# Optimization experiments

Measured on AMD Instinct MI355X. Metric: run time of the kernel, lower is better.

## Reference

```python
import jax, jax.numpy as jnp
import numpy as np

HIDDEN = 2048
HEADS = 16
HEAD_DIM = HIDDEN // HEADS  # 128
ROPE_BASE = 10000.0
RMS_EPS = 1e-6
MINUS_INF = -10000.0


def rms_norm(x, w):
    xf = x.astype(jnp.float32)
    var = jnp.mean(xf * xf, axis=-1, keepdims=True)
    return w * (x * jax.lax.rsqrt(var + RMS_EPS))


def rotate_half(x):
    x1, x2 = jnp.split(x, 2, axis=-1)
    return jnp.concatenate((-x2, x1), axis=-1)


def rope_tables(seq_len, dtype):
    inv_freq = 1.0 / (ROPE_BASE ** (jnp.arange(0, HEAD_DIM, 2, dtype=jnp.float32) / HEAD_DIM))
    t = jnp.arange(seq_len, dtype=jnp.float32)
    freqs = jnp.einsum('i,j->ij', t, inv_freq)           # [S, D/2]
    emb = jnp.concatenate((freqs, freqs), axis=-1)       # [S, D]
    return jnp.cos(emb).astype(dtype), jnp.sin(emb).astype(dtype)


def setup_inputs() -> dict:
    key = jax.random.key(0)
    ks = jax.random.split(key, 6)
    B, S, H = 2, 2048, HIDDEN
    x = jax.random.normal(ks[0], (B, S, H), dtype=jnp.float32) * 0.5
    norm_w = jnp.ones((H,), dtype=jnp.float32)
    scale = 0.02
    wq = jax.random.normal(ks[1], (H, H), dtype=jnp.float32) * scale
    wk = jax.random.normal(ks[2], (H, H), dtype=jnp.float32) * scale
    wv = jax.random.normal(ks[3], (H, H), dtype=jnp.float32) * scale
    wo = jax.random.normal(ks[4], (H, H), dtype=jnp.float32) * scale
    position_ids = jnp.broadcast_to(jnp.arange(S, dtype=jnp.int32), (B, S))
    return {"x": x, "norm_w": norm_w, "wq": wq, "wk": wk, "wv": wv,
            "wo": wo, "position_ids": position_ids}


def reference(x, norm_w, wq, wk, wv, wo, position_ids):
    B, S, H = x.shape
    h = rms_norm(x, norm_w)
    # torch Linear: y = h @ W.T, weight is [out, in]
    def proj(w):
        return jnp.einsum('bsd,od->bso', h, w).reshape(B, S, HEADS, HEAD_DIM).transpose(0, 2, 1, 3)
    q, k, v = proj(wq), proj(wk), proj(wv)  # [B, Hh, S, D]
    cos, sin = rope_tables(S, x.dtype)
    cos = cos[position_ids][:, None]  # [B, 1, S, D]
    sin = sin[position_ids][:, None]
    q = q * cos + rotate_half(q) * sin
    k = k * cos + rotate_half(k) * sin
    scores = jnp.einsum('bhqd,bhkd->bhqk', q, k) / jnp.sqrt(jnp.float32(HEAD_DIM))
    causal = jnp.tril(jnp.ones((S, S), dtype=bool))
    scores = scores + jnp.where(causal, 0.0, MINUS_INF).astype(scores.dtype)
    probs = jax.nn.softmax(scores, axis=-1)
    ctx = jnp.einsum('bhqk,bhkd->bhqd', probs, v)          # [B, Hh, S, D]
    ctx = ctx.transpose(0, 2, 1, 3).reshape(B, S, H)
    out = jnp.einsum('bsd,od->bso', ctx, wo)
    return out
```

## Files before the change

### kernel.cpp

```cpp
#include <hip/hip_runtime.h>
#include <hip/hip_bf16.h>
#include <stdint.h>

#define S_LEN   2048
#define BATCH   2
#define HID     2048
#define NHEADS  16
#define HDIM    128
#define ROWS    (BATCH * S_LEN)
#define QKS     4096
#define ATT_SCALE 0.08838834764831843f
#define LOG2E     1.4426950408889634f

typedef __attribute__((ext_vector_type(8))) short s16x8;
typedef __attribute__((ext_vector_type(4))) float f32x4;

#define GLL16(gp, lp)                                                          \
  __builtin_amdgcn_global_load_lds(                                            \
      (__attribute__((address_space(1))) void*)(gp),                           \
      (__attribute__((address_space(3))) void*)(lp), 16, 0, 0)

__device__ __forceinline__ float bf2f(unsigned short u) {
  union { unsigned int i; float f; } v; v.i = ((unsigned int)u) << 16; return v.f;
}
__device__ __forceinline__ unsigned short f2bf(float f) {
  union { float f; unsigned int i; } v; v.f = f;
  unsigned int i = v.i;
  return (unsigned short)((i + 0x7FFFu + ((i >> 16) & 1u)) >> 16);
}
__device__ __forceinline__ void store_out(unsigned short* p, float v) { *p = f2bf(v); }
__device__ __forceinline__ void store_out(float* p, float v) { *p = v; }

__global__ __launch_bounds__(256) void cast4_kernel(const float* __restrict__ w0,
                                                    const float* __restrict__ w1,
                                                    const float* __restrict__ w2,
                                                    const float* __restrict__ w3,
                                                    unsigned short* __restrict__ dqkv,
                                                    unsigned short* __restrict__ dwo) {
  const int which = blockIdx.y;
  const float* src = (which == 0) ? w0 : (which == 1) ? w1 : (which == 2) ? w2 : w3;
  unsigned short* dst = (which < 3) ? dqkv + (size_t)which * HID * HID : dwo;
  int i = blockIdx.x * 256 + threadIdx.x;
  float4 v = ((const float4*)src)[i];
  ushort4 o;
  o.x = f2bf(v.x); o.y = f2bf(v.y); o.z = f2bf(v.z); o.w = f2bf(v.w);
  ((ushort4*)dst)[i] = o;
}

__global__ __launch_bounds__(256) void rmsnorm_kernel(const float* __restrict__ x,
                                                      const float* __restrict__ w,
                                                      unsigned short* __restrict__ h) {
  int row = blockIdx.x;
  int t = threadIdx.x;
  const float4* xr4 = (const float4*)(x + (size_t)row * HID);
  float4 a = xr4[t], b = xr4[t + 256];
  float ss = a.x*a.x + a.y*a.y + a.z*a.z + a.w*a.w
           + b.x*b.x + b.y*b.y + b.z*b.z + b.w*b.w;
#pragma unroll
  for (int off = 32; off >= 1; off >>= 1) ss += __shfl_xor(ss, off, 64);
  __shared__ float red[4];
  if ((t & 63) == 0) red[t >> 6] = ss;
  __syncthreads();
  float tot = red[0] + red[1] + red[2] + red[3];
  float rs = rsqrtf(tot * (1.0f / (float)HID) + 1e-6f);
  const float4* w4 = (const float4*)w;
  float4 wa = w4[t], wb = w4[t + 256];
  ushort4 oa, ob;
  oa.x = f2bf(a.x * wa.x * rs); oa.y = f2bf(a.y * wa.y * rs);
  oa.z = f2bf(a.z * wa.z * rs); oa.w = f2bf(a.w * wa.w * rs);
  ob.x = f2bf(b.x * wb.x * rs); ob.y = f2bf(b.y * wb.y * rs);
  ob.z = f2bf(b.z * wb.z * rs); ob.w = f2bf(b.w * wb.w * rs);
  ushort4* hr = (ushort4*)(h + (size_t)row * HID);
  hr[t] = oa; hr[t + 256] = ob;
}

__global__ void rope_tab_kernel(float* __restrict__ cost, float* __restrict__ sint) {
  int s = blockIdx.x, j = threadIdx.x;
  float inv = powf(10000.0f, -((float)j) / 64.0f);
  float ang = (float)s * inv;
  cost[s * 64 + j] = cosf(ang);
  sint[s * 64 + j] = sinf(ang);
}

__global__ __launch_bounds__(256) void rope_kernel(const int* __restrict__ pos_ids,
                                                   const float* __restrict__ cost,
                                                   const float* __restrict__ sint,
                                                   unsigned short* __restrict__ qk) {
  int row = blockIdx.x;
  int p = pos_ids[row];
  int t = threadIdx.x;
  int head = t >> 4;
  int j0 = (t & 15) * 4;
  size_t base = (size_t)row * QKS + head * HDIM;
  float4 c = *(const float4*)(cost + p * 64 + j0);
  float4 s = *(const float4*)(sint + p * 64 + j0);
#pragma unroll
  for (int which = 0; which < 2; which++) {
    unsigned short* ptr = qk + base + which * HID;
    float sc = which ? 1.0f : (ATT_SCALE * LOG2E);
    ushort4 v1 = *(ushort4*)(ptr + j0);
    ushort4 v2 = *(ushort4*)(ptr + 64 + j0);
    ushort4 o1, o2;
    o1.x = f2bf((bf2f(v1.x) * c.x - bf2f(v2.x) * s.x) * sc);
    o1.y = f2bf((bf2f(v1.y) * c.y - bf2f(v2.y) * s.y) * sc);
    o1.z = f2bf((bf2f(v1.z) * c.z - bf2f(v2.z) * s.z) * sc);
    o1.w = f2bf((bf2f(v1.w) * c.w - bf2f(v2.w) * s.w) * sc);
    o2.x = f2bf((bf2f(v2.x) * c.x + bf2f(v1.x) * s.x) * sc);
    o2.y = f2bf((bf2f(v2.y) * c.y + bf2f(v1.y) * s.y) * sc);
    o2.z = f2bf((bf2f(v2.z) * c.z + bf2f(v1.z) * s.z) * sc);
    o2.w = f2bf((bf2f(v2.w) * c.w + bf2f(v1.w) * s.w) * sc);
    *(ushort4*)(ptr + j0) = o1;
    *(ushort4*)(ptr + 64 + j0) = o2;
  }
}

#define SH(kt, bi, kk2) {                                                      \
    const unsigned short* sa_ = aQ + (size_t)(kt) * 64 + (kk2) * 32;           \
    const unsigned short* sb_ = bQ + (size_t)(kt) * 64 + (kk2) * 32;           \
    char* da_ = qsm + ((bi) * 2 + (kk2)) * 32768 + tid * 16;                   \
    GLL16(sa_, da_);                                                           \
    GLL16(sa_ + (size_t)128 * K, da_ + 8192);                                  \
    GLL16(sb_, da_ + 16384);                                                   \
    GLL16(sb_ + (size_t)128 * K, da_ + 16384 + 8192);                          \
  }

__global__ __launch_bounds__(512, 2) void gemm_qk_kernel(const unsigned short* __restrict__ A,
                                                         const unsigned short* __restrict__ B,
                                                         unsigned short* __restrict__ C,
                                                         int K, int N) {
  __shared__ __align__(16) unsigned short Qsm[2][2][2][256 * 32];
  const int bm = blockIdx.y, bn = blockIdx.x;
  const int tid = threadIdx.x;
  const int w = tid >> 6, wr = w >> 2, wc = w & 3;
  const int l = tid & 63, g = l >> 4, r = l & 15;
  const int KT = K >> 6;

  const int srow = tid >> 2;
  const int sg = (tid & 3) ^ ((tid >> 2) & 3) ^ ((tid >> 4) & 3);
  const unsigned short* aQ = A + (size_t)(bm * 256 + srow) * K + sg * 8;
  const unsigned short* bQ = B + (size_t)(bn * 256 + srow) * K + sg * 8;
  char* const qsm = (char*)Qsm;

  f32x4 zero = {0.f, 0.f, 0.f, 0.f};
  f32x4 acc[8][4];
#pragma unroll
  for (int mi = 0; mi < 8; mi++)
#pragma unroll
    for (int ni = 0; ni < 4; ni++) acc[mi][ni] = zero;

  const int ro = ((g ^ (r & 3) ^ ((r >> 2) & 3)) << 4);
  const int aOff = (wr * 128 + r) * 64 + ro;
  const int bOff = 16384 + (wc * 64 + r) * 64 + ro;

  SH(0, 0, 0); SH(0, 0, 1);

  for (int kt = 0; kt < KT; ++kt) {
    const int buf = kt & 1;
    const bool more = (kt + 1 < KT);
    const char* l0 = qsm + (buf * 2 + 0) * 32768;
    const char* l1 = qsm + (buf * 2 + 1) * 32768;

    asm volatile("s_waitcnt vmcnt(4)" ::: "memory");
    __builtin_amdgcn_s_barrier();
    __builtin_amdgcn_sched_barrier(0);
    s16x8 a[4], b[4];
#pragma unroll
    for (int ni = 0; ni < 4; ni++) b[ni] = *(const s16x8*)(l0 + bOff + ni * 1024);
#pragma unroll
    for (int i = 0; i < 4; i++) a[i] = *(const s16x8*)(l0 + aOff + i * 1024);
    if (more) SH(kt + 1, buf ^ 1, 0);
    __builtin_amdgcn_s_setprio(1);
#pragma unroll
    for (int ni = 0; ni < 4; ni++)
#pragma unroll
      for (int i = 0; i < 4; i++)
        acc[i][ni] = __builtin_amdgcn_mfma_f32_16x16x32_bf16(a[i], b[ni], acc[i][ni], 0, 0, 0);
    __builtin_amdgcn_s_setprio(0);

    s16x8 a2[4];
#pragma unroll
    for (int i = 0; i < 4; i++) a2[i] = *(const s16x8*)(l0 + aOff + (4 + i) * 1024);
    __builtin_amdgcn_s_setprio(1);
#pragma unroll
    for (int ni = 0; ni < 4; ni++)
#pragma unroll
      for (int i = 0; i < 4; i++)
        acc[4 + i][ni] = __builtin_amdgcn_mfma_f32_16x16x32_bf16(a2[i], b[ni], acc[4 + i][ni], 0, 0, 0);
    __builtin_amdgcn_s_setprio(0);

    if (more) { asm volatile("s_waitcnt vmcnt(4)" ::: "memory"); }
    else      { asm volatile("s_waitcnt vmcnt(0)" ::: "memory"); }
    __builtin_amdgcn_s_barrier();
    __builtin_amdgcn_sched_barrier(0);
#pragma unroll
    for (int ni = 0; ni < 4; ni++) b[ni] = *(const s16x8*)(l1 + bOff + ni * 1024);
#pragma unroll
    for (int i = 0; i < 4; i++) a[i] = *(const s16x8*)(l1 + aOff + i * 1024);
    if (more) SH(kt + 1, buf ^ 1, 1);
    __builtin_amdgcn_s_setprio(1);
#pragma unroll
    for (int ni = 0; ni < 4; ni++)
#pragma unroll
      for (int i = 0; i < 4; i++)
        acc[i][ni] = __builtin_amdgcn_mfma_f32_16x16x32_bf16(a[i], b[ni], acc[i][ni], 0, 0, 0);
    __builtin_amdgcn_s_setprio(0);

#pragma unroll
    for (int i = 0; i < 4; i++) a2[i] = *(const s16x8*)(l1 + aOff + (4 + i) * 1024);
    __builtin_amdgcn_s_setprio(1);
#pragma unroll
    for (int ni = 0; ni < 4; ni++)
#pragma unroll
      for (int i = 0; i < 4; i++)
        acc[4 + i][ni] = __builtin_amdgcn_mfma_f32_16x16x32_bf16(a2[i], b[ni], acc[4 + i][ni], 0, 0, 0);
    __builtin_amdgcn_s_setprio(0);
  }

#pragma unroll
  for (int mi = 0; mi < 8; mi++)
#pragma unroll
    for (int ni = 0; ni < 4; ni++) {
      const int crow = bm * 256 + wr * 128 + mi * 16 + g * 4;
      const int ccol = bn * 256 + wc * 64 + ni * 16 + r;
#pragma unroll
      for (int j = 0; j < 4; j++)
        store_out(&C[(size_t)(crow + j) * N + ccol], acc[mi][ni][j]);
    }
}
#undef SH

#define SA(kt, bi) {                                                           \
    const unsigned short* s_ = aS + (size_t)(kt) * 64;                         \
    char* d_ = (char*)Ab[bi] + tid * 16;                                       \
    GLL16(s_, d_);                                                             \
    GLL16(s_ + (size_t)64 * K, d_ + 8192);                                     \
  }
#define SB(kt, bi, hf) {                                                       \
    const unsigned short* s_ = bS + (size_t)(hf) * 128 * K + (size_t)(kt) * 64;\
    char* d_ = (char*)Bb[bi] + (hf) * 16384 + tid * 16;                        \
    GLL16(s_, d_);                                                             \
    GLL16(s_ + (size_t)64 * K, d_ + 8192);                                     \
  }

template <typename OutT, int NI, bool VT_OUT>
__global__ __launch_bounds__(512, 1) void gemm8_kernel(const unsigned short* __restrict__ A,
                                                       const unsigned short* __restrict__ B,
                                                       OutT* __restrict__ C, int K, int N) {
  __shared__ __align__(16) unsigned short Ab[3][128 * 64];
  __shared__ __align__(16) unsigned short Bb[3][NI * 64 * 64];
  const int bm = blockIdx.y, bn = blockIdx.x;
  const int tid = threadIdx.x;
  const int w = tid >> 6, wr = w >> 2, wc = w & 3;
  const int l = tid & 63, g = l >> 4, r = l & 15;
  const int KT = K >> 6;

  const int srow = tid >> 3;
  const int sgr = (tid & 7) ^ (srow & 7);
  const unsigned short* aS = A + (size_t)(bm * 128 + srow) * K + sgr * 8;
  const unsigned short* bS = B + (size_t)(bn * (NI * 64) + srow) * K + sgr * 8;

  f32x4 zero = {0.f, 0.f, 0.f, 0.f};
  f32x4 acc[4][NI];
#pragma unroll
  for (int mi = 0; mi < 4; mi++)
#pragma unroll
    for (int ni = 0; ni < NI; ni++) acc[mi][ni] = zero;

  const int swx = (r & 7) << 4;
  const int ks0 = (g << 4) ^ swx;
  const int ks1 = ((4 | g) << 4) ^ swx;
  const int aOff = (wr * 64 + r) * 128;
  const int bOff = (wc * (NI * 16) + r) * 128;

  SA(0, 0); SB(0, 0, 0); if (NI == 4) SB(0, 0, 1);
  SA(1, 1); SB(1, 1, 0); if (NI == 4) SB(1, 1, 1);

  int cur = 0;
  for (int kt = 0; kt < KT; ++kt) {
    const int b2 = (cur >= 1) ? cur - 1 : cur + 2;
    if (kt == KT - 1)      { asm volatile("s_waitcnt vmcnt(0)" ::: "memory"); }
    else if (NI == 4)      { asm volatile("s_waitcnt vmcnt(6)" ::: "memory"); }
    else                   { asm volatile("s_waitcnt vmcnt(4)" ::: "memory"); }
    __builtin_amdgcn_s_barrier();
    __builtin_amdgcn_sched_barrier(0);
    const char* lA = (const char*)Ab[cur];
    const char* lB = (const char*)Bb[cur];
    const bool more = (kt + 2 < KT);

    s16x8 a[4][2], b[NI][2];
#pragma unroll
    for (int mi = 0; mi < 4; mi++) {
      a[mi][0] = *(const s16x8*)(lA + aOff + mi * 2048 + ks0);
      a[mi][1] = *(const s16x8*)(lA + aOff + mi * 2048 + ks1);
    }
#pragma unroll
    for (int ni = 0; ni < NI / 2; ni++) {
      b[ni][0] = *(const s16x8*)(lB + bOff + ni * 2048 + ks0);
      b[ni][1] = *(const s16x8*)(lB + bOff + ni * 2048 + ks1);
    }
    if (more) { SA(kt + 2, b2); if (NI == 4) SB(kt + 2, b2, 0); }
    __builtin_amdgcn_s_setprio(1);
#pragma unroll
    for (int kk = 0; kk < 2; kk++)
#pragma unroll
      for (int ni = 0; ni < NI / 2; ni++)
#pragma unroll
        for (int mi = 0; mi < 4; mi++)
          acc[mi][ni] = __builtin_amdgcn_mfma_f32_16x16x32_bf16(a[mi][kk], b[ni][kk], acc[mi][ni], 0, 0, 0);
    __builtin_amdgcn_s_setprio(0);
    __builtin_amdgcn_sched_barrier(0);

#pragma unroll
    for (int ni = NI / 2; ni < NI; ni++) {
      b[ni][0] = *(const s16x8*)(lB + bOff + ni * 2048 + ks0);
      b[ni][1] = *(const s16x8*)(lB + bOff + ni * 2048 + ks1);
    }
    if (more) { if (NI == 4) { SB(kt + 2, b2, 1); } else { SB(kt + 2, b2, 0); } }
    __builtin_amdgcn_s_setprio(1);
#pragma unroll
    for (int kk = 0; kk < 2; kk++)
#pragma unroll
      for (int ni = NI / 2; ni < NI; ni++)
#pragma unroll
        for (int mi = 0; mi < 4; mi++)
          acc[mi][ni] = __builtin_amdgcn_mfma_f32_16x16x32_bf16(a[mi][kk], b[ni][kk], acc[mi][ni], 0, 0, 0);
    __builtin_amdgcn_s_setprio(0);
    cur = (cur == 2) ? 0 : cur + 1;
  }

#pragma unroll
  for (int mi = 0; mi < 4; mi++)
#pragma unroll
    for (int ni = 0; ni < NI; ni++) {
      const int crow = bm * 128 + wr * 64 + mi * 16 + g * 4;
      const int ccol = bn * (NI * 64) + wc * (NI * 16) + ni * 16 + r;
      if constexpr (VT_OUT) {
        const int bidx = crow >> 11;
        const int s0 = crow & (S_LEN - 1);
        const int vrow = (bidx * 16 + (ccol >> 7)) * 128 + (ccol & 127);
        ushort4 o;
        o.x = f2bf(acc[mi][ni][0]); o.y = f2bf(acc[mi][ni][1]);
        o.z = f2bf(acc[mi][ni][2]); o.w = f2bf(acc[mi][ni][3]);
        *(ushort4*)((unsigned short*)C + (size_t)vrow * S_LEN + s0) = o;
      } else {
#pragma unroll
        for (int j = 0; j < 4; j++)
          store_out(&C[(size_t)(crow + j) * N + ccol], acc[mi][ni][j]);
      }
    }
}

__global__ __launch_bounds__(256, 2) void attn_kernel(const unsigned short* __restrict__ QK,
                                                      const unsigned short* __restrict__ VT,
                                                      unsigned short* __restrict__ O) {
  __shared__ __align__(16) unsigned short Ksm[2][64 * 128];
  __shared__ __align__(16) unsigned short VTsm[2][128 * 64];
  __shared__ __align__(16) unsigned short Psm[4 * 16 * 64];
  const int bid = blockIdx.x;
  const int grp = bid & 7, idx = bid >> 3;
  const int p = idx >> 2;
  const int bh = (grp << 2) | (idx & 3);
  const int b = bh >> 4, hd = bh & 15;
  const int tid = threadIdx.x, w = tid >> 6, l = tid & 63, g = l >> 4, r = l & 15;

  const int cK = tid & 15, rowK = tid >> 4;
  const unsigned short* kp_base = QK + (size_t)(b * S_LEN + rowK) * QKS + HID + hd * HDIM
                                  + ((cK ^ (rowK & 7)) << 3);
  const int cV = tid & 7, dV = tid >> 3;
  const unsigned short* vp_base = VT + (size_t)(bh * 128 + dV) * S_LEN + ((cV ^ (dV & 7)) << 3);
  char* const ksm0 = (char*)Ksm;
  char* const vtsm0 = (char*)VTsm;
  char* const psm_w = (char*)Psm + w * 2048;
  const int pswz = (r & 7) << 4;
  f32x4 zero = {0.f, 0.f, 0.f, 0.f};

#define STAGE(kt, bufi)                                                        \
  {                                                                            \
    const unsigned short* kp_ = kp_base + (size_t)((kt) * 64) * QKS;           \
    const unsigned short* vp_ = vp_base + (kt) * 64;                           \
    char* kd_ = ksm0 + (bufi) * 16384;                                         \
    char* vd_ = vtsm0 + (bufi) * 16384;                                        \
    GLL16(kp_,                      kd_ + tid * 16);                           \
    GLL16(kp_ + (size_t)16 * QKS,   kd_ + (tid + 256) * 16);                   \
    GLL16(kp_ + (size_t)32 * QKS,   kd_ + (tid + 512) * 16);                   \
    GLL16(kp_ + (size_t)48 * QKS,   kd_ + (tid + 768) * 16);                   \
    GLL16(vp_,                      vd_ + tid * 16);                           \
    GLL16(vp_ + (size_t)32 * S_LEN, vd_ + (tid + 256) * 16);                   \
    GLL16(vp_ + (size_t)64 * S_LEN, vd_ + (tid + 512) * 16);                   \
    GLL16(vp_ + (size_t)96 * S_LEN, vd_ + (tid + 768) * 16);                   \
  }

  for (int pass = 0; pass < 2; pass++) {
    const int qt = pass ? p : 31 - p;
    const int qbs = qt * 64 + w * 16;

    const unsigned short* qp = QK + (size_t)(b * S_LEN + qbs + r) * QKS + hd * HDIM;
    s16x8 qf[4];
#pragma unroll
    for (int ks = 0; ks < 4; ks++) qf[ks] = *(const s16x8*)(qp + ks * 32 + g * 8);

    float mreg = -1e30f, lregp = 0.f;
    f32x4 oacc[8];
#pragma unroll
    for (int di = 0; di < 8; di++) oacc[di] = zero;

    if (pass) __builtin_amdgcn_s_barrier();
    const int nt = qt + 1;
    STAGE(0, 0);

    for (int kt2 = 0; kt2 < nt; kt2++) {
      const int buf = kt2 & 1;
      asm volatile("s_waitcnt vmcnt(0)" ::: "memory");
      __builtin_amdgcn_s_barrier();
      __builtin_amdgcn_sched_barrier(0);
      if (kt2 + 1 < nt) STAGE(kt2 + 1, buf ^ 1);

      const char* ksm_c = ksm0 + buf * 16384;
      const char* vtsm_c = vtsm0 + buf * 16384;

      f32x4 sacc[4];
#pragma unroll
      for (int ni = 0; ni < 4; ni++) sacc[ni] = zero;
#pragma unroll
      for (int ni = 0; ni < 4; ni++) {
        const int krow = ni * 16 + r;
        const int swz = (krow & 7) << 4;
        const char* kb2 = ksm_c + krow * 256;
#pragma unroll
        for (int ks = 0; ks < 4; ks++) {
          s16x8 kf = *(const s16x8*)(kb2 + ((ks * 64 + g * 16) ^ swz));
          sacc[ni] = __builtin_amdgcn_mfma_f32_16x16x32_bf16(kf, qf[ks], sacc[ni], 0, 0, 0);
        }
      }

      if (kt2 == qt) {
#pragma unroll
        for (int ni = 0; ni < 4; ni++)
#pragma unroll
          for (int jj = 0; jj < 4; jj++)
            if ((kt2 * 64 + ni * 16 + g * 4 + jj) > (qbs + r)) sacc[ni][jj] = -1e30f;
      }

      float m0 = fmaxf(fmaxf(sacc[0][0], sacc[0][1]), fmaxf(sacc[0][2], sacc[0][3]));
      float m1 = fmaxf(fmaxf(sacc[1][0], sacc[1][1]), fmaxf(sacc[1][2], sacc[1][3]));
      float m2 = fmaxf(fmaxf(sacc[2][0], sacc[2][1]), fmaxf(sacc[2][2], sacc[2][3]));
      float m3 = fmaxf(fmaxf(sacc[3][0], sacc[3][1]), fmaxf(sacc[3][2], sacc[3][3]));
      float mx = fmaxf(fmaxf(m0, m1), fmaxf(m2, m3));
      mx = fmaxf(mx, __shfl_xor(mx, 16, 64));
      mx = fmaxf(mx, __shfl_xor(mx, 32, 64));

      if (__any(mx > mreg + 8.0f)) {
        float mn = fmaxf(mreg, mx);
        float corr = exp2f(mreg - mn);
        mreg = mn;
        lregp *= corr;
#pragma unroll
        for (int di = 0; di < 8; di++) oacc[di] = oacc[di] * corr;
      }

#pragma unroll
      for (int ni = 0; ni < 4; ni++)
#pragma unroll
        for (int jj = 0; jj < 4; jj++) sacc[ni][jj] = exp2f(sacc[ni][jj] - mreg);
      float s0 = (sacc[0][0] + sacc[0][1]) + (sacc[0][2] + sacc[0][3]);
      float s1 = (sacc[1][0] + sacc[1][1]) + (sacc[1][2] + sacc[1][3]);
      float s2 = (sacc[2][0] + sacc[2][1]) + (sacc[2][2] + sacc[2][3]);
      float s3 = (sacc[3][0] + sacc[3][1]) + (sacc[3][2] + sacc[3][3]);
      lregp += (s0 + s1) + (s2 + s3);

#pragma unroll
      for (int ni = 0; ni < 4; ni++) {
        unsigned int pk01, pk23;
        asm("v_cvt_pk_bf16_f32 %0, %1, %2" : "=v"(pk01) : "v"(sacc[ni][0]), "v"(sacc[ni][1]));
        asm("v_cvt_pk_bf16_f32 %0, %1, %2" : "=v"(pk23) : "v"(sacc[ni][2]), "v"(sacc[ni][3]));
        uint2 pk; pk.x = pk01; pk.y = pk23;
        *(uint2*)(psm_w + ((r * 128 + ni * 32 + g * 8) ^ pswz)) = pk;
      }

#pragma unroll
      for (int ksl = 0; ksl < 2; ksl++) {
        s16x8 pb = *(const s16x8*)(psm_w + ((r * 128 + ksl * 64 + g * 16) ^ pswz));
        const int kgran = ksl * 4 + g;
#pragma unroll
        for (int di = 0; di < 8; di++) {
          const int d = di * 16 + r;
          s16x8 vf = *(const s16x8*)(vtsm_c + d * 128 + ((kgran ^ (d & 7)) << 4));
          oacc[di] = __builtin_amdgcn_mfma_f32_16x16x32_bf16(vf, pb, oacc[di], 0, 0, 0);
        }
      }
    }

    float lsum = lregp;
    lsum += __shfl_xor(lsum, 16, 64);
    lsum += __shfl_xor(lsum, 32, 64);
    const float inv = 1.0f / lsum;
    unsigned short* orow = O + (size_t)(b * S_LEN + qbs + r) * HID + hd * HDIM;
#pragma unroll
    for (int di = 0; di < 8; di++) {
      ushort4 o;
      o.x = f2bf(oacc[di][0] * inv); o.y = f2bf(oacc[di][1] * inv);
      o.z = f2bf(oacc[di][2] * inv); o.w = f2bf(oacc[di][3] * inv);
      *(ushort4*)(orow + di * 16 + g * 4) = o;
    }
  }
#undef STAGE
}

extern "C" void kernel_launch(void* const* d_in, const int* in_sizes, int n_in,
                              void* d_out, int out_size, void* d_ws, size_t ws_size,
                              hipStream_t stream) {
  const float* x      = (const float*)d_in[0];
  const float* norm_w = (const float*)d_in[1];
  const float* wq     = (const float*)d_in[2];
  const float* wk     = (const float*)d_in[3];
  const float* wv     = (const float*)d_in[4];
  const float* wo     = (const float*)d_in[5];
  const int*   pos    = (const int*)d_in[6];
  float* out = (float*)d_out;

  char* ws = (char*)d_ws;
  const size_t WQKV_B = (size_t)3 * HID * HID * 2;
  const size_t WO_B   = (size_t)HID * HID * 2;
  const size_t H_B    = (size_t)ROWS * HID * 2;
  const size_t QK_B   = (size_t)ROWS * QKS * 2;

  unsigned short* wqkvb = (unsigned short*)(ws);
  unsigned short* vt    = (unsigned short*)(ws);
  unsigned short* wob   = (unsigned short*)(ws + WQKV_B);
  unsigned short* h     = (unsigned short*)(ws + WQKV_B + WO_B);
  unsigned short* qk    = (unsigned short*)(ws + WQKV_B + WO_B + H_B);
  float* cost = (float*)(ws + WQKV_B + WO_B + H_B + QK_B);
  float* sint = cost + (size_t)S_LEN * 64;

  dim3 cgrid(HID * HID / 4 / 256, 4);
  cast4_kernel<<<cgrid, 256, 0, stream>>>(wq, wk, wv, wo, wqkvb, wob);
  rope_tab_kernel<<<S_LEN, 64, 0, stream>>>(cost, sint);
  rmsnorm_kernel<<<ROWS, 256, 0, stream>>>(x, norm_w, h);

  dim3 qkgrid(2 * HID / 256, ROWS / 256);
  gemm_qk_kernel<<<qkgrid, 512, 0, stream>>>(h, wqkvb, qk, HID, QKS);

  dim3 vgrid(HID / 256, ROWS / 128);
  gemm8_kernel<unsigned short, 4, true><<<vgrid, 512, 0, stream>>>(
      h, wqkvb + (size_t)2 * HID * HID, vt, HID, S_LEN);

  rope_kernel<<<ROWS, 256, 0, stream>>>(pos, cost, sint, qk);

  attn_kernel<<<512, 256, 0, stream>>>(qk, vt, h );

  dim3 ogrid(HID / 256, ROWS / 128);
  gemm8_kernel<float, 4, false><<<ogrid, 512, 0, stream>>>(h, wob, out, HID, HID);
}
```

Measured before the change: 255.3 us.

## Load V fragments straight into registers and launch one query tile per block

The attention kernel no longer stages the transposed V tile through double-buffered shared memory. Each wave now reads its V fragments directly from global memory into registers, issued right after the K prefetch, and feeds them to the PV MFMAs. Separately, the two-pass pairing of a long and a short query tile per block is replaced by 1024 blocks that each handle a single query tile, ordered heaviest first, and the launch-bounds occupancy hint is dropped. This frees shared memory and removes the V staging traffic, at the cost of four-fold redundant global (L2) reads of V across the waves in a block. It also adds more register pressure and leaves load balance to the hardware scheduler.

```diff
diff --git a/kernel.cpp b/kernel.cpp
--- a/kernel.cpp
+++ b/kernel.cpp
@@ -350,160 +350,149 @@
     }
 }
 
-__global__ __launch_bounds__(256, 2) void attn_kernel(const unsigned short* __restrict__ QK,
-                                                      const unsigned short* __restrict__ VT,
-                                                      unsigned short* __restrict__ O) {
+__global__ __launch_bounds__(256) void attn_kernel(const unsigned short* __restrict__ QK,
+                                                   const unsigned short* __restrict__ VT,
+                                                   unsigned short* __restrict__ O) {
   __shared__ __align__(16) unsigned short Ksm[2][64 * 128];
-  __shared__ __align__(16) unsigned short VTsm[2][128 * 64];
   __shared__ __align__(16) unsigned short Psm[4 * 16 * 64];
   const int bid = blockIdx.x;
   const int grp = bid & 7, idx = bid >> 3;
-  const int p = idx >> 2;
+  const int qt = 31 - (idx >> 2);
   const int bh = (grp << 2) | (idx & 3);
   const int b = bh >> 4, hd = bh & 15;
   const int tid = threadIdx.x, w = tid >> 6, l = tid & 63, g = l >> 4, r = l & 15;
+  const int qbs = qt * 64 + w * 16;
+
+  const unsigned short* qp = QK + (size_t)(b * S_LEN + qbs + r) * QKS + hd * HDIM;
+  s16x8 qf[4];
+#pragma unroll
+  for (int ks = 0; ks < 4; ks++) qf[ks] = *(const s16x8*)(qp + ks * 32 + g * 8);
+
+  float mreg = -1e30f, lregp = 0.f;
+  f32x4 zero = {0.f, 0.f, 0.f, 0.f};
+  f32x4 oacc[8];
+#pragma unroll
+  for (int di = 0; di < 8; di++) oacc[di] = zero;
 
   const int cK = tid & 15, rowK = tid >> 4;
   const unsigned short* kp_base = QK + (size_t)(b * S_LEN + rowK) * QKS + HID + hd * HDIM
                                   + ((cK ^ (rowK & 7)) << 3);
-  const int cV = tid & 7, dV = tid >> 3;
-  const unsigned short* vp_base = VT + (size_t)(bh * 128 + dV) * S_LEN + ((cV ^ (dV & 7)) << 3);
+  const unsigned short* vgp = VT + (size_t)(bh * 128 + r) * S_LEN + g * 8;
   char* const ksm0 = (char*)Ksm;
-  char* const vtsm0 = (char*)VTsm;
   char* const psm_w = (char*)Psm + w * 2048;
   const int pswz = (r & 7) << 4;
-  f32x4 zero = {0.f, 0.f, 0.f, 0.f};
 
 #define STAGE(kt, bufi)                                                        \
   {                                                                            \
     const unsigned short* kp_ = kp_base + (size_t)((kt) * 64) * QKS;           \
-    const unsigned short* vp_ = vp_base + (kt) * 64;                           \
     char* kd_ = ksm0 + (bufi) * 16384;                                         \
-    char* vd_ = vtsm0 + (bufi) * 16384;                                        \
     GLL16(kp_,                      kd_ + tid * 16);                           \
     GLL16(kp_ + (size_t)16 * QKS,   kd_ + (tid + 256) * 16);                   \
     GLL16(kp_ + (size_t)32 * QKS,   kd_ + (tid + 512) * 16);                   \
     GLL16(kp_ + (size_t)48 * QKS,   kd_ + (tid + 768) * 16);                   \
-    GLL16(vp_,                      vd_ + tid * 16);                           \
-    GLL16(vp_ + (size_t)32 * S_LEN, vd_ + (tid + 256) * 16);                   \
-    GLL16(vp_ + (size_t)64 * S_LEN, vd_ + (tid + 512) * 16);                   \
-    GLL16(vp_ + (size_t)96 * S_LEN, vd_ + (tid + 768) * 16);                   \
-  }
-
-  for (int pass = 0; pass < 2; pass++) {
-    const int qt = pass ? p : 31 - p;
-    const int qbs = qt * 64 + w * 16;
-
-    const unsigned short* qp = QK + (size_t)(b * S_LEN + qbs + r) * QKS + hd * HDIM;
-    s16x8 qf[4];
-#pragma unroll
-    for (int ks = 0; ks < 4; ks++) qf[ks] = *(const s16x8*)(qp + ks * 32 + g * 8);
-
-    float mreg = -1e30f, lregp = 0.f;
-    f32x4 oacc[8];
-#pragma unroll
-    for (int di = 0; di < 8; di++) oacc[di] = zero;
-
-    if (pass) __builtin_amdgcn_s_barrier();
-    const int nt = qt + 1;
-    STAGE(0, 0);
-
-    for (int kt2 = 0; kt2 < nt; kt2++) {
-      const int buf = kt2 & 1;
-      asm volatile("s_waitcnt vmcnt(0)" ::: "memory");
-      __builtin_amdgcn_s_barrier();
-      __builtin_amdgcn_sched_barrier(0);
-      if (kt2 + 1 < nt) STAGE(kt2 + 1, buf ^ 1);
-
-      const char* ksm_c = ksm0 + buf * 16384;
-      const char* vtsm_c = vtsm0 + buf * 16384;
-
-      f32x4 sacc[4];
-#pragma unroll
-      for (int ni = 0; ni < 4; ni++) sacc[ni] = zero;
-#pragma unroll
-      for (int ni = 0; ni < 4; ni++) {
-        const int krow = ni * 16 + r;
-        const int swz = (krow & 7) << 4;
-        const char* kb2 = ksm_c + krow * 256;
-#pragma unroll
-        for (int ks = 0; ks < 4; ks++) {
-          s16x8 kf = *(const s16x8*)(kb2 + ((ks * 64 + g * 16) ^ swz));
-          sacc[ni] = __builtin_amdgcn_mfma_f32_16x16x32_bf16(kf, qf[ks], sacc[ni], 0, 0, 0);
-        }
+  }
+
+  const int nt = qt + 1;
+  STAGE(0, 0);
+
+  for (int kt2 = 0; kt2 < nt; kt2++) {
+    const int buf = kt2 & 1;
+    asm volatile("s_waitcnt vmcnt(0)" ::: "memory");
+    __builtin_amdgcn_s_barrier();
+    __builtin_amdgcn_sched_barrier(0);
+    if (kt2 + 1 < nt) STAGE(kt2 + 1, buf ^ 1);
+
+    const unsigned short* vrow = vgp + kt2 * 64;
+    s16x8 vfr[2][8];
+#pragma unroll
+    for (int ksl = 0; ksl < 2; ksl++)
+#pragma unroll
+      for (int di = 0; di < 8; di++)
+        vfr[ksl][di] = *(const s16x8*)(vrow + (size_t)di * 16 * S_LEN + ksl * 32);
+
+    const char* ksm_c = ksm0 + buf * 16384;
+
+    f32x4 sacc[4];
+#pragma unroll
+    for (int ni = 0; ni < 4; ni++) sacc[ni] = zero;
+#pragma unroll
+    for (int ni = 0; ni < 4; ni++) {
+      const int krow = ni * 16 + r;
+      const int swz = (krow & 7) << 4;
+      const char* kb2 = ksm_c + krow * 256;
+#pragma unroll
+      for (int ks = 0; ks < 4; ks++) {
+        s16x8 kf = *(const s16x8*)(kb2 + ((ks * 64 + g * 16) ^ swz));
+        sacc[ni] = __builtin_amdgcn_mfma_f32_16x16x32_bf16(kf, qf[ks], sacc[ni], 0, 0, 0);
       }
-
-      if (kt2 == qt) {
-#pragma unroll
-        for (int ni = 0; ni < 4; ni++)
-#pragma unroll
-          for (int jj = 0; jj < 4; jj++)
-            if ((kt2 * 64 + ni * 16 + g * 4 + jj) > (qbs + r)) sacc[ni][jj] = -1e30f;
-      }
-
-      float m0 = fmaxf(fmaxf(sacc[0][0], sacc[0][1]), fmaxf(sacc[0][2], sacc[0][3]));
-      float m1 = fmaxf(fmaxf(sacc[1][0], sacc[1][1]), fmaxf(sacc[1][2], sacc[1][3]));
-      float m2 = fmaxf(fmaxf(sacc[2][0], sacc[2][1]), fmaxf(sacc[2][2], sacc[2][3]));
-      float m3 = fmaxf(fmaxf(sacc[3][0], sacc[3][1]), fmaxf(sacc[3][2], sacc[3][3]));
-      float mx = fmaxf(fmaxf(m0, m1), fmaxf(m2, m3));
-      mx = fmaxf(mx, __shfl_xor(mx, 16, 64));
-      mx = fmaxf(mx, __shfl_xor(mx, 32, 64));
-
-      if (__any(mx > mreg + 8.0f)) {
-        float mn = fmaxf(mreg, mx);
-        float corr = exp2f(mreg - mn);
-        mreg = mn;
-        lregp *= corr;
-#pragma unroll
-        for (int di = 0; di < 8; di++) oacc[di] = oacc[di] * corr;
-      }
-
+    }
+
+    if (kt2 == qt) {
 #pragma unroll
       for (int ni = 0; ni < 4; ni++)
 #pragma unroll
-        for (int jj = 0; jj < 4; jj++) sacc[ni][jj] = exp2f(sacc[ni][jj] - mreg);
-      float s0 = (sacc[0][0] + sacc[0][1]) + (sacc[0][2] + sacc[0][3]);
-      float s1 = (sacc[1][0] + sacc[1][1]) + (sacc[1][2] + sacc[1][3]);
-      float s2 = (sacc[2][0] + sacc[2][1]) + (sacc[2][2] + sacc[2][3]);
-      float s3 = (sacc[3][0] + sacc[3][1]) + (sacc[3][2] + sacc[3][3]);
-      lregp += (s0 + s1) + (s2 + s3);
-
-#pragma unroll
-      for (int ni = 0; ni < 4; ni++) {
-        unsigned int pk01, pk23;
-        asm("v_cvt_pk_bf16_f32 %0, %1, %2" : "=v"(pk01) : "v"(sacc[ni][0]), "v"(sacc[ni][1]));
-        asm("v_cvt_pk_bf16_f32 %0, %1, %2" : "=v"(pk23) : "v"(sacc[ni][2]), "v"(sacc[ni][3]));
-        uint2 pk; pk.x = pk01; pk.y = pk23;
-        *(uint2*)(psm_w + ((r * 128 + ni * 32 + g * 8) ^ pswz)) = pk;
-      }
-
-#pragma unroll
-      for (int ksl = 0; ksl < 2; ksl++) {
-        s16x8 pb = *(const s16x8*)(psm_w + ((r * 128 + ksl * 64 + g * 16) ^ pswz));
-        const int kgran = ksl * 4 + g;
-#pragma unroll
-        for (int di = 0; di < 8; di++) {
-          const int d = di * 16 + r;
-          s16x8 vf = *(const s16x8*)(vtsm_c + d * 128 + ((kgran ^ (d & 7)) << 4));
-          oacc[di] = __builtin_amdgcn_mfma_f32_16x16x32_bf16(vf, pb, oacc[di], 0, 0, 0);
-        }
-      }
-    }
-
-    float lsum = lregp;
-    lsum += __shfl_xor(lsum, 16, 64);
-    lsum += __shfl_xor(lsum, 32, 64);
-    const float inv = 1.0f / lsum;
-    unsigned short* orow = O + (size_t)(b * S_LEN + qbs + r) * HID + hd * HDIM;
-#pragma unroll
-    for (int di = 0; di < 8; di++) {
-      ushort4 o;
-      o.x = f2bf(oacc[di][0] * inv); o.y = f2bf(oacc[di][1] * inv);
-      o.z = f2bf(oacc[di][2] * inv); o.w = f2bf(oacc[di][3] * inv);
-      *(ushort4*)(orow + di * 16 + g * 4) = o;
+        for (int jj = 0; jj < 4; jj++)
+          if ((kt2 * 64 + ni * 16 + g * 4 + jj) > (qbs + r)) sacc[ni][jj] = -1e30f;
+    }
+
+    float m0 = fmaxf(fmaxf(sacc[0][0], sacc[0][1]), fmaxf(sacc[0][2], sacc[0][3]));
+    float m1 = fmaxf(fmaxf(sacc[1][0], sacc[1][1]), fmaxf(sacc[1][2], sacc[1][3]));
+    float m2 = fmaxf(fmaxf(sacc[2][0], sacc[2][1]), fmaxf(sacc[2][2], sacc[2][3]));
+    float m3 = fmaxf(fmaxf(sacc[3][0], sacc[3][1]), fmaxf(sacc[3][2], sacc[3][3]));
+    float mx = fmaxf(fmaxf(m0, m1), fmaxf(m2, m3));
+    mx = fmaxf(mx, __shfl_xor(mx, 16, 64));
+    mx = fmaxf(mx, __shfl_xor(mx, 32, 64));
+
+    if (__any(mx > mreg + 8.0f)) {
+      float mn = fmaxf(mreg, mx);
+      float corr = exp2f(mreg - mn);
+      mreg = mn;
+      lregp *= corr;
+#pragma unroll
+      for (int di = 0; di < 8; di++) oacc[di] = oacc[di] * corr;
+    }
+
+#pragma unroll
+    for (int ni = 0; ni < 4; ni++)
+#pragma unroll
+      for (int jj = 0; jj < 4; jj++) sacc[ni][jj] = exp2f(sacc[ni][jj] - mreg);
+    float s0 = (sacc[0][0] + sacc[0][1]) + (sacc[0][2] + sacc[0][3]);
+    float s1 = (sacc[1][0] + sacc[1][1]) + (sacc[1][2] + sacc[1][3]);
+    float s2 = (sacc[2][0] + sacc[2][1]) + (sacc[2][2] + sacc[2][3]);
+    float s3 = (sacc[3][0] + sacc[3][1]) + (sacc[3][2] + sacc[3][3]);
+    lregp += (s0 + s1) + (s2 + s3);
+
+#pragma unroll
+    for (int ni = 0; ni < 4; ni++) {
+      unsigned int pk01, pk23;
+      asm("v_cvt_pk_bf16_f32 %0, %1, %2" : "=v"(pk01) : "v"(sacc[ni][0]), "v"(sacc[ni][1]));
+      asm("v_cvt_pk_bf16_f32 %0, %1, %2" : "=v"(pk23) : "v"(sacc[ni][2]), "v"(sacc[ni][3]));
+      uint2 pk; pk.x = pk01; pk.y = pk23;
+      *(uint2*)(psm_w + ((r * 128 + ni * 32 + g * 8) ^ pswz)) = pk;
+    }
+
+#pragma unroll
+    for (int ksl = 0; ksl < 2; ksl++) {
+      s16x8 pb = *(const s16x8*)(psm_w + ((r * 128 + ksl * 64 + g * 16) ^ pswz));
+#pragma unroll
+      for (int di = 0; di < 8; di++)
+        oacc[di] = __builtin_amdgcn_mfma_f32_16x16x32_bf16(vfr[ksl][di], pb, oacc[di], 0, 0, 0);
     }
   }
 #undef STAGE
+
+  float lsum = lregp;
+  lsum += __shfl_xor(lsum, 16, 64);
+  lsum += __shfl_xor(lsum, 32, 64);
+  const float inv = 1.0f / lsum;
+  unsigned short* orow = O + (size_t)(b * S_LEN + qbs + r) * HID + hd * HDIM;
+#pragma unroll
+  for (int di = 0; di < 8; di++) {
+    ushort4 o;
+    o.x = f2bf(oacc[di][0] * inv); o.y = f2bf(oacc[di][1] * inv);
+    o.z = f2bf(oacc[di][2] * inv); o.w = f2bf(oacc[di][3] * inv);
+    *(ushort4*)(orow + di * 16 + g * 4) = o;
+  }
 }
 
 extern "C" void kernel_launch(void* const* d_in, const int* in_sizes, int n_in,
@@ -546,7 +535,7 @@
 
   rope_kernel<<<ROWS, 256, 0, stream>>>(pos, cost, sint, qk);
 
-  attn_kernel<<<512, 256, 0, stream>>>(qk, vt, h );
+  attn_kernel<<<1024, 256, 0, stream>>>(qk, vt, h );
 
   dim3 ogrid(HID / 256, ROWS / 128);
   gemm8_kernel<float, 4, false><<<ogrid, 512, 0, stream>>>(h, wob, out, HID, HID);
```

New measurement: 329.3 us. +29.0%, slower.
